# Kernel tuning notes

Hardware: AMD Instinct MI355X
Metric: run time of the kernel (lower is better)

Reference implementation:

```python
import math
import jax, jax.numpy as jnp
import numpy as np

B, C, H, W = 8, 128, 128, 128

def _cosine_basis(n):
    pos = (jnp.arange(n, dtype=jnp.float32) + 0.5) / n          # [n]
    freq = jnp.arange(n, dtype=jnp.float32)[:, None]            # [n,1]
    basis = jnp.cos(freq * pos[None, :] * math.pi) * math.sqrt(2.0 / n)
    return basis.at[0, :].multiply(1.0 / math.sqrt(2.0))        # [n,n]


def setup_inputs() -> dict:
    key = jax.random.key(0)
    ks = jax.random.split(key, 12)
    s = 0.02
    return {
        "x":        jax.random.normal(ks[0], (B, C, H, W), jnp.float32),
        "dw_w":     jax.random.normal(ks[1], (C, 1, 3, 3), jnp.float32) * s,
        "dw_b":     jnp.zeros((C,), jnp.float32),
        "in_w":     jax.random.normal(ks[2], (2 * C, C), jnp.float32) * s,
        "in_b":     jnp.zeros((2 * C,), jnp.float32),
        "out_w":    jax.random.normal(ks[3], (C, C), jnp.float32) * s,
        "out_b":    jnp.zeros((C,), jnp.float32),
        "ln_w":     jnp.ones((C,), jnp.float32),
        "ln_b":     jnp.zeros((C,), jnp.float32),
        "ph_w":     jax.random.normal(ks[4], (C, C), jnp.float32) * s,
        "ph_b":     jnp.zeros((C,), jnp.float32),
        "wave_speed": jnp.ones((1,), jnp.float32),
        "damping":    jnp.full((1,), 0.1, jnp.float32),
        "freq_embed": jax.random.normal(ks[5], (H, W, C), jnp.float32) * s,
    }


def reference(x, dw_w, dw_b, in_w, in_b, out_w, out_b, ln_w, ln_b,
              ph_w, ph_b, wave_speed, damping, freq_embed):
    # depthwise 3x3 conv (groups=C), padding=1
    mixed = jax.lax.conv_general_dilated(
        x, dw_w, window_strides=(1, 1), padding=((1, 1), (1, 1)),
        dimension_numbers=("NCHW", "OIHW", "NCHW"), feature_group_count=C)
    mixed = mixed + dw_b[None, :, None, None]
    mixed = jnp.transpose(mixed, (0, 2, 3, 1))                  # [B,H,W,C]

    proj = mixed @ in_w.T + in_b                                # [B,H,W,2C]
    carrier, gate = jnp.split(proj, 2, axis=-1)

    cos_h = _cosine_basis(H)
    cos_w = _cosine_basis(W)
    # DCT-II along H then W
    spectral = jnp.einsum("bhwc,nh->bnwc", carrier, cos_h)
    spectral = jnp.einsum("bnwc,mw->bnmc", spectral, cos_w)     # [B,H,W,C] (freq)

    # phase modulation (base_resolution == H == W, so no resize)
    phase = jax.nn.gelu(freq_embed @ ph_w.T + ph_b, approximate=False)  # [H,W,C]
    wave_phase = wave_speed * phase                             # broadcast [H,W,C]
    vel_scale = jnp.sin(wave_phase) / jnp.maximum(jnp.abs(wave_speed), 1e-6)
    modulated = (jnp.cos(wave_phase) + vel_scale * (1.0 + 0.5 * damping)) * spectral

    # inverse DCT
    fused = jnp.einsum("bnmc,wm->bnwc", modulated, cos_w.T)
    fused = jnp.einsum("bnwc,hn->bhwc", fused, cos_h.T)         # [B,H,W,C]

    # LayerNorm over channels
    mu = jnp.mean(fused, axis=-1, keepdims=True)
    var = jnp.mean(jnp.square(fused - mu), axis=-1, keepdims=True)
    fused = (fused - mu) / jnp.sqrt(var + 1e-5) * ln_w + ln_b

    fused = fused * jax.nn.silu(gate)
    out = fused @ out_w.T + out_b                               # [B,H,W,C]
    return jnp.transpose(out, (0, 3, 1, 2))                     # [B,C,H,W]
```

## Files before the change

### kernel.cpp

```cpp
#include <hip/hip_runtime.h>
#include <math.h>

#ifndef M_PI
#define M_PI 3.14159265358979323846
#endif

typedef float fx4 __attribute__((ext_vector_type(4)));
typedef __bf16 bf16x8 __attribute__((ext_vector_type(8)));
typedef __bf16 bf16x4 __attribute__((ext_vector_type(4)));

__device__ __forceinline__ unsigned short f2bf(float f){
  union { float f; unsigned u; } v; v.f = f;
  unsigned r = v.u + 0x7FFFu + ((v.u >> 16) & 1u);
  return (unsigned short)(r >> 16);
}
__device__ __forceinline__ float bf2f(unsigned short u){
  union { unsigned u; float f; } v; v.u = ((unsigned)u) << 16;
  return v.f;
}
__device__ __forceinline__ int swz(int row, int colbyte){
  return row*256 + (colbyte ^ ((row & 7) << 4));
}

template<typename FA, typename FB>
__device__ __forceinline__ void run_gemm(FA la, FB lb, fx4 (&acc)[4][4]){
  bf16x8 a[2][4], b[2][4];
  #pragma unroll
  for (int mi=0;mi<4;mi++){ a[0][mi]=la(mi,0); b[0][mi]=lb(mi,0); }
  #pragma unroll
  for (int ks=0; ks<4; ks++){
    int cur = ks&1, nxt = cur^1;
    if (ks<3){
      #pragma unroll
      for (int mi=0;mi<4;mi++){ a[nxt][mi]=la(mi,ks+1); b[nxt][mi]=lb(mi,ks+1); }
    }
    #pragma unroll
    for (int mi=0;mi<4;mi++)
      #pragma unroll
      for (int ni=0;ni<4;ni++)
        acc[mi][ni] = __builtin_amdgcn_mfma_f32_16x16x32_bf16(a[cur][mi], b[cur][ni], acc[mi][ni], 0, 0, 0);
  }
}

template<typename FA0, typename FA1, typename FB>
__device__ __forceinline__ void run_pair_sharedB(FA0 la0, FA1 la1, FB lb,
                                                 fx4 (&acc0)[4][4], fx4 (&acc1)[4][4]){
  bf16x8 a0[2][4], a1[2][4], b[2][4];
  #pragma unroll
  for (int mi=0;mi<4;mi++){ a0[0][mi]=la0(mi,0); a1[0][mi]=la1(mi,0); b[0][mi]=lb(mi,0); }
  #pragma unroll
  for (int ks=0; ks<4; ks++){
    int cur = ks&1, nxt = cur^1;
    if (ks<3){
      #pragma unroll
      for (int mi=0;mi<4;mi++){ a0[nxt][mi]=la0(mi,ks+1); a1[nxt][mi]=la1(mi,ks+1); b[nxt][mi]=lb(mi,ks+1); }
    }
    #pragma unroll
    for (int mi=0;mi<4;mi++)
      #pragma unroll
      for (int ni=0;ni<4;ni++){
        acc0[mi][ni] = __builtin_amdgcn_mfma_f32_16x16x32_bf16(a0[cur][mi], b[cur][ni], acc0[mi][ni], 0, 0, 0);
        acc1[mi][ni] = __builtin_amdgcn_mfma_f32_16x16x32_bf16(a1[cur][mi], b[cur][ni], acc1[mi][ni], 0, 0, 0);
      }
  }
}

template<typename FA, typename FB0, typename FB1>
__device__ __forceinline__ void run_pair_sharedA(FA la, FB0 lb0, FB1 lb1,
                                                 fx4 (&acc0)[4][4], fx4 (&acc1)[4][4]){
  bf16x8 a[2][4], b0[2][4], b1[2][4];
  #pragma unroll
  for (int mi=0;mi<4;mi++){ a[0][mi]=la(mi,0); b0[0][mi]=lb0(mi,0); b1[0][mi]=lb1(mi,0); }
  #pragma unroll
  for (int ks=0; ks<4; ks++){
    int cur = ks&1, nxt = cur^1;
    if (ks<3){
      #pragma unroll
      for (int mi=0;mi<4;mi++){ a[nxt][mi]=la(mi,ks+1); b0[nxt][mi]=lb0(mi,ks+1); b1[nxt][mi]=lb1(mi,ks+1); }
    }
    #pragma unroll
    for (int mi=0;mi<4;mi++)
      #pragma unroll
      for (int ni=0;ni<4;ni++){
        acc0[mi][ni] = __builtin_amdgcn_mfma_f32_16x16x32_bf16(a[cur][mi], b0[cur][ni], acc0[mi][ni], 0, 0, 0);
        acc1[mi][ni] = __builtin_amdgcn_mfma_f32_16x16x32_bf16(a[cur][mi], b1[cur][ni], acc1[mi][ni], 0, 0, 0);
      }
  }
}

__global__ __launch_bounds__(256) void k1_prep_cast_conv(
    const float* __restrict__ in_w, const float* __restrict__ ph_w,
    const float* __restrict__ out_w, const float* __restrict__ fe,
    const float* __restrict__ x, const float* __restrict__ dw_w,
    const float* __restrict__ dw_b,
    unsigned short* __restrict__ basis_bf, unsigned short* __restrict__ basisT_bf,
    unsigned short* __restrict__ ph_w_bf, unsigned short* __restrict__ in_w_bf,
    unsigned short* __restrict__ out_w_bf, unsigned short* __restrict__ feb,
    unsigned short* __restrict__ conv)
{
  int blk = blockIdx.x;
  int t = threadIdx.x;
  if (blk < 128){
    if (t >= 128) return;
    int n = blk, h = t;
    double arg = (double)(n*(2*h+1)) * (M_PI/256.0);
    double v = cos(arg) * 0.125;
    if (n==0) v *= 0.7071067811865476;
    unsigned short bv = f2bf((float)v);
    basis_bf[n*128+h]  = bv;
    basisT_bf[h*128+n] = bv;
    ph_w_bf[n*128+h]  = f2bf(ph_w[n*128+h]);
    in_w_bf[n*128+h]        = f2bf(in_w[n*128+h]);
    in_w_bf[(n+128)*128+h]  = f2bf(in_w[(n+128)*128+h]);
    out_w_bf[n*128+h]       = f2bf(out_w[n*128+h]);
    return;
  }
  if (blk < 1152){
    int idx = (blk-128)*256 + t;
    const float* s = fe + (size_t)idx*8;
    float4 f0 = *(const float4*)s;
    float4 f1 = *(const float4*)(s+4);
    unsigned short o[8];
    o[0]=f2bf(f0.x); o[1]=f2bf(f0.y); o[2]=f2bf(f0.z); o[3]=f2bf(f0.w);
    o[4]=f2bf(f1.x); o[5]=f2bf(f1.y); o[6]=f2bf(f1.z); o[7]=f2bf(f1.w);
    *(int4*)(feb + (size_t)idx*8) = *(const int4*)o;
    return;
  }
  {
    int bb = blk - 1152;
    int plane = bb >> 2, band = bb & 3;
    int c = plane & 127;
    const float* xp = x + (size_t)plane*16384;
    unsigned short* op = conv + (size_t)plane*16384;
    const float* kw = dw_w + c*9;
    float k0=kw[0],k1=kw[1],k2=kw[2],k3=kw[3],k4=kw[4],k5=kw[5],k6=kw[6],k7=kw[7],k8=kw[8];
    float bias = dw_b[c];
    int q = t & 31;
    int w0 = q*4;
    int rg = t >> 5;
    int h0 = band*32 + rg*4;
    bool le = (q==0), re = (q==31);
    float4 fA, fB, fC; float lA,rA,lB,rB,lC,rC;
    #define LOADROW(hh, f, l, r) { \
      int hc = (hh)<0 ? 0 : ((hh)>127 ? 127 : (hh)); \
      f = *(const float4*)(xp + hc*128 + w0); \
      float lu = __shfl_up(f.w, 1, 32); \
      float rd = __shfl_down(f.x, 1, 32); \
      l = le ? 0.f : lu; \
      r = re ? 0.f : rd; \
      if ((hh)<0 || (hh)>127){ f = make_float4(0.f,0.f,0.f,0.f); l=0.f; r=0.f; } \
    }
    LOADROW(h0-1, fA,lA,rA);
    LOADROW(h0,   fB,lB,rB);
    #pragma unroll
    for (int i=0;i<4;i++){
      LOADROW(h0+1+i, fC,lC,rC);
      float4 o;
      o.x = bias; o.y = bias; o.z = bias; o.w = bias;
      o.x = fmaf(k0,lA,  fmaf(k1,fA.x, fmaf(k2,fA.y, o.x)));
      o.y = fmaf(k0,fA.x,fmaf(k1,fA.y, fmaf(k2,fA.z, o.y)));
      o.z = fmaf(k0,fA.y,fmaf(k1,fA.z, fmaf(k2,fA.w, o.z)));
      o.w = fmaf(k0,fA.z,fmaf(k1,fA.w, fmaf(k2,rA,   o.w)));
      o.x = fmaf(k3,lB,  fmaf(k4,fB.x, fmaf(k5,fB.y, o.x)));
      o.y = fmaf(k3,fB.x,fmaf(k4,fB.y, fmaf(k5,fB.z, o.y)));
      o.z = fmaf(k3,fB.y,fmaf(k4,fB.z, fmaf(k5,fB.w, o.z)));
      o.w = fmaf(k3,fB.z,fmaf(k4,fB.w, fmaf(k5,rB,   o.w)));
      o.x = fmaf(k6,lC,  fmaf(k7,fC.x, fmaf(k8,fC.y, o.x)));
      o.y = fmaf(k6,fC.x,fmaf(k7,fC.y, fmaf(k8,fC.z, o.y)));
      o.z = fmaf(k6,fC.y,fmaf(k7,fC.z, fmaf(k8,fC.w, o.z)));
      o.w = fmaf(k6,fC.z,fmaf(k7,fC.w, fmaf(k8,rC,   o.w)));
      bf16x4 v;
      v[0]=(__bf16)o.x; v[1]=(__bf16)o.y; v[2]=(__bf16)o.z; v[3]=(__bf16)o.w;
      *(bf16x4*)(op + (size_t)(h0+i)*128 + w0) = v;
      fA=fB; lA=lB; rA=rB;
      fB=fC; lB=lC; rB=rC;
    }
    #undef LOADROW
  }
}

__global__ __launch_bounds__(512) void k2_inproj_projk(
  const unsigned short* __restrict__ conv, const unsigned short* __restrict__ in_w_bf,
  const float* __restrict__ in_b, unsigned short* __restrict__ carrier,
  unsigned short* __restrict__ gate,
  const unsigned short* __restrict__ feb, const unsigned short* __restrict__ ph_w_bf,
  float* __restrict__ projT)
{
  int blk = blockIdx.x;
  int t = threadIdx.x;
  if (blk >= 1024){
    if (t >= 256) return;
    int r0 = (blk - 1024) * 128;
    int l = t & 63, wid = t >> 6;
    int wm = wid >> 1, wn = wid & 1;
    int lr = l & 15, lk = (l>>4)*8, ld4 = (l>>4)*4;
    fx4 acc[4][4];
    #pragma unroll
    for (int i=0;i<4;i++) for (int j=0;j<4;j++) acc[i][j] = (fx4){0.f,0.f,0.f,0.f};
    run_gemm(
      [&](int mi,int ks)->bf16x8{ return *(const bf16x8*)(feb + (size_t)(r0 + wm*64+mi*16+lr)*128 + ks*32+lk); },
      [&](int ni,int ks)->bf16x8{ return *(const bf16x8*)(ph_w_bf + (size_t)(wn*64+ni*16+lr)*128 + ks*32+lk); },
      acc);
    #pragma unroll
    for (int mi=0;mi<4;mi++)
      #pragma unroll
      for (int ni=0;ni<4;ni++){
        int c = wn*64 + ni*16 + lr;
        int r = r0 + wm*64 + mi*16 + ld4;
        *(fx4*)(projT + (size_t)c*16384 + r) = acc[mi][ni];
      }
    return;
  }
  __shared__ char A[32768];
  int b = blk>>7, h = blk&127;
  const unsigned short* C = conv + (size_t)b*2097152 + h*128;
  {
    int wl = t & 63, grp = t >> 6;
    #pragma unroll
    for (int p=0;p<2;p++){
      int w = wl + 64*p;
      #pragma unroll
      for (int q=0;q<4;q++){
        int c0 = (q*8 + grp)*4;
        ushort4 v;
        v.x = C[(size_t)(c0+0)*16384 + w];
        v.y = C[(size_t)(c0+1)*16384 + w];
        v.z = C[(size_t)(c0+2)*16384 + w];
        v.w = C[(size_t)(c0+3)*16384 + w];
        *(ushort4*)(A + swz(w, c0*2)) = v;
      }
    }
  }
  __syncthreads();
  int l = t & 63, wid = t >> 6;
  int wm = wid >> 2, wn = wid & 3;
  int lr = l & 15, lk = (l>>4)*8, ld4 = (l>>4)*4;
  fx4 acc[4][4];
  #pragma unroll
  for (int i=0;i<4;i++) for (int j=0;j<4;j++) acc[i][j] = (fx4){0.f,0.f,0.f,0.f};
  run_gemm(
    [&](int mi,int ks)->bf16x8{ return *(const bf16x8*)(A + swz(wm*64+mi*16+lr, (ks*32+lk)*2)); },
    [&](int ni,int ks)->bf16x8{ return *(const bf16x8*)(in_w_bf + (size_t)(wn*64+ni*16+lr)*128 + ks*32+lk); },
    acc);
  __syncthreads();
  if (wn < 2){
    #pragma unroll
    for (int mi=0;mi<4;mi++)
      #pragma unroll
      for (int ni=0;ni<4;ni++){
        int n = wn*64 + ni*16 + lr;
        int w0 = wm*64 + mi*16 + ld4;
        float bias = in_b[n];
        bf16x4 v;
        v[0]=(__bf16)(acc[mi][ni][0]+bias); v[1]=(__bf16)(acc[mi][ni][1]+bias);
        v[2]=(__bf16)(acc[mi][ni][2]+bias); v[3]=(__bf16)(acc[mi][ni][3]+bias);
        *(bf16x4*)(carrier + (size_t)(b*128+n)*16384 + h*128 + w0) = v;
      }
  } else {
    #pragma unroll
    for (int mi=0;mi<4;mi++)
      #pragma unroll
      for (int ni=0;ni<4;ni++){
        int n = wn*64 + ni*16 + lr;
        int c = n - 128;
        int w0 = wm*64 + mi*16 + ld4;
        float bias = in_b[n];
        #pragma unroll
        for (int r=0;r<4;r++){
          float v = acc[mi][ni][r] + bias;
          float s = v / (1.0f + __expf(-v));
          *(__bf16*)(A + swz(w0+r, c*2)) = (__bf16)s;
        }
      }
  }
  __syncthreads();
  {
    unsigned short* gout = gate + ((size_t)(b*128+h))*16384;
    int w = t >> 2, cq = (t & 3) * 32;
    #pragma unroll
    for (int i=0;i<4;i++){
      int c0 = cq + i*8;
      int4 v = *(const int4*)(A + swz(w, c0*2));
      *(int4*)(gout + w*128 + c0) = v;
    }
  }
}

__global__ __launch_bounds__(256) void modfin_kernel(
  const float* __restrict__ projT, const float* __restrict__ ph_b,
  const float* __restrict__ wave_speed, const float* __restrict__ damping,
  float* __restrict__ modT)
{
  int blk = blockIdx.x;
  int c = blk >> 4, qb = blk & 15;
  int t = threadIdx.x;
  int q = qb*8 + (t>>5);
  int p0 = (t & 31)*4;
  float ws0 = wave_speed[0];
  float dmp = damping[0];
  float inv = 1.0f / fmaxf(fabsf(ws0), 1e-6f);
  float dampf = 1.0f + 0.5f*dmp;
  float bc = ph_b[c];
  const float* src = projT + (size_t)c*16384 + q;
  float o[4];
  #pragma unroll
  for (int i=0;i<4;i++){
    float v = src[(size_t)(p0+i)*128] + bc;
    float g = 0.5f*v*(1.0f + erff(v*0.70710678118f));
    float wp = ws0*g;
    o[i] = __cosf(wp) + __sinf(wp)*inv*dampf;
  }
  *(float4*)(modT + ((size_t)c*128 + q)*128 + p0) = make_float4(o[0],o[1],o[2],o[3]);
}

__global__ __launch_bounds__(256) void wave_kernel(
  const unsigned short* __restrict__ carrier,
  const unsigned short* __restrict__ basis,
  const unsigned short* __restrict__ basisT,
  const float* __restrict__ modT,
  unsigned short* __restrict__ fused)
{
  __shared__ char U0[32768];
  __shared__ char U1[32768];
  int blk = blockIdx.x;
  int c = blk & 127;
  const unsigned short* X0 = carrier + (size_t)blk*16384;
  const unsigned short* X1 = carrier + (size_t)(blk+512)*16384;
  unsigned short* F0 = fused + (size_t)blk*16384;
  unsigned short* F1 = fused + (size_t)(blk+512)*16384;
  int t = threadIdx.x;
  int l = t & 63, wid = t >> 6;
  int wm = wid >> 1, wn = wid & 1;
  int lr = l & 15, lk = (l>>4)*8, ld4 = (l>>4)*4;
  fx4 acc0[4][4], acc1[4][4];

  #define ZACC { _Pragma("unroll") for (int i=0;i<4;i++) _Pragma("unroll") for (int j=0;j<4;j++){ acc0[i][j]=(fx4){0.f,0.f,0.f,0.f}; acc1[i][j]=(fx4){0.f,0.f,0.f,0.f}; } }
  #define TSTORE(BUF0, BUF1) { \
    _Pragma("unroll") for (int mi=0;mi<4;mi++) \
      _Pragma("unroll") for (int ni=0;ni<4;ni++){ \
        int rr = wn*64 + ni*16 + lr, cc = wm*64 + mi*16 + ld4; \
        bf16x4 v0, v1; \
        v0[0]=(__bf16)acc0[mi][ni][0]; v0[1]=(__bf16)acc0[mi][ni][1]; \
        v0[2]=(__bf16)acc0[mi][ni][2]; v0[3]=(__bf16)acc0[mi][ni][3]; \
        v1[0]=(__bf16)acc1[mi][ni][0]; v1[1]=(__bf16)acc1[mi][ni][1]; \
        v1[2]=(__bf16)acc1[mi][ni][2]; v1[3]=(__bf16)acc1[mi][ni][3]; \
        *(bf16x4*)(BUF0 + swz(rr, cc*2)) = v0; \
        *(bf16x4*)(BUF1 + swz(rr, cc*2)) = v1; \
      } }

  ZACC;
  run_pair_sharedB(
    [&](int mi,int ks)->bf16x8{ return *(const bf16x8*)(X0 + (size_t)(wm*64+mi*16+lr)*128 + ks*32+lk); },
    [&](int mi,int ks)->bf16x8{ return *(const bf16x8*)(X1 + (size_t)(wm*64+mi*16+lr)*128 + ks*32+lk); },
    [&](int ni,int ks)->bf16x8{ return *(const bf16x8*)(basis + (size_t)(wn*64+ni*16+lr)*128 + ks*32+lk); },
    acc0, acc1);
  TSTORE(U0, U1);
  __syncthreads();

  ZACC;
  run_pair_sharedA(
    [&](int mi,int ks)->bf16x8{ return *(const bf16x8*)(basis + (size_t)(wm*64+mi*16+lr)*128 + ks*32+lk); },
    [&](int ni,int ks)->bf16x8{ return *(const bf16x8*)(U0 + swz(wn*64+ni*16+lr, (ks*32+lk)*2)); },
    [&](int ni,int ks)->bf16x8{ return *(const bf16x8*)(U1 + swz(wn*64+ni*16+lr, (ks*32+lk)*2)); },
    acc0, acc1);
  {
    const float* Mc = modT + (size_t)c*16384;
    #pragma unroll
    for (int mi=0;mi<4;mi++)
      #pragma unroll
      for (int ni=0;ni<4;ni++){
        int n0 = wm*64 + mi*16 + ld4, m = wn*64 + ni*16 + lr;
        fx4 mv = *(const fx4*)(Mc + (size_t)m*128 + n0);
        acc0[mi][ni] *= mv;
        acc1[mi][ni] *= mv;
      }
  }
  __syncthreads();
  TSTORE(U0, U1);
  __syncthreads();

  ZACC;
  run_pair_sharedB(
    [&](int mi,int ks)->bf16x8{ return *(const bf16x8*)(U0 + swz(wm*64+mi*16+lr, (ks*32+lk)*2)); },
    [&](int mi,int ks)->bf16x8{ return *(const bf16x8*)(U1 + swz(wm*64+mi*16+lr, (ks*32+lk)*2)); },
    [&](int ni,int ks)->bf16x8{ return *(const bf16x8*)(basisT + (size_t)(wn*64+ni*16+lr)*128 + ks*32+lk); },
    acc0, acc1);
  __syncthreads();
  TSTORE(U0, U1);
  __syncthreads();

  ZACC;
  run_pair_sharedA(
    [&](int mi,int ks)->bf16x8{ return *(const bf16x8*)(basisT + (size_t)(wm*64+mi*16+lr)*128 + ks*32+lk); },
    [&](int ni,int ks)->bf16x8{ return *(const bf16x8*)(U0 + swz(wn*64+ni*16+lr, (ks*32+lk)*2)); },
    [&](int ni,int ks)->bf16x8{ return *(const bf16x8*)(U1 + swz(wn*64+ni*16+lr, (ks*32+lk)*2)); },
    acc0, acc1);
  #pragma unroll
  for (int mi=0;mi<4;mi++)
    #pragma unroll
    for (int ni=0;ni<4;ni++){
      int hh = wn*64 + ni*16 + lr, w0 = wm*64 + mi*16 + ld4;
      bf16x4 v0, v1;
      v0[0]=(__bf16)acc0[mi][ni][0]; v0[1]=(__bf16)acc0[mi][ni][1];
      v0[2]=(__bf16)acc0[mi][ni][2]; v0[3]=(__bf16)acc0[mi][ni][3];
      v1[0]=(__bf16)acc1[mi][ni][0]; v1[1]=(__bf16)acc1[mi][ni][1];
      v1[2]=(__bf16)acc1[mi][ni][2]; v1[3]=(__bf16)acc1[mi][ni][3];
      *(bf16x4*)(F0 + hh*128 + w0) = v0;
      *(bf16x4*)(F1 + hh*128 + w0) = v1;
    }
  #undef ZACC
  #undef TSTORE
}

__global__ __launch_bounds__(256) void final_kernel(
  const unsigned short* __restrict__ fused, const unsigned short* __restrict__ gate,
  const unsigned short* __restrict__ out_w_bf, const float* __restrict__ out_b,
  const float* __restrict__ ln_w, const float* __restrict__ ln_b,
  float* __restrict__ out)
{
  __shared__ char Fl[32768];
  __shared__ char Al[32768];
  __shared__ float red[256], red2[256];
  __shared__ float mu[128], rs[128];
  int blk = blockIdx.x; int b = blk>>7, h = blk&127;
  const unsigned short* Fsrc = fused + (size_t)b*2097152 + h*128;
  const unsigned short* G = gate + (size_t)blk*16384;
  int t = threadIdx.x;
  {
    int c = t>>1, wq = (t&1)*64;
    #pragma unroll
    for (int i=0;i<8;i++){
      int w0 = wq + i*8;
      int4 v = *(const int4*)(Fsrc + (size_t)c*16384 + w0);
      *(int4*)(Fl + swz(c, w0*2)) = v;
    }
  }
  __syncthreads();
  {
    int w = t&127, half = t>>7;
    float s=0.f, q=0.f;
    for (int i=0;i<64;i++){
      int c = half*64 + i;
      float f = bf2f(*(const unsigned short*)(Fl + swz(c, w*2)));
      s += f; q = fmaf(f,f,q);
    }
    red[t]=s; red2[t]=q;
  }
  __syncthreads();
  if (t < 128){
    float ss = red[t]+red[t+128], qq = red2[t]+red2[t+128];
    float m = ss*(1.f/128.f);
    float var = qq*(1.f/128.f) - m*m;
    mu[t]=m; rs[t]=rsqrtf(var+1e-5f);
  }
  __syncthreads();
  {
    int w = t>>1, cq = (t&1)*64;
    float m_ = mu[w], r_ = rs[w];
    #pragma unroll
    for (int i=0;i<8;i++){
      int c0 = cq + i*8;
      ushort4 g0 = *(const ushort4*)(G + (size_t)w*128 + c0);
      ushort4 g1 = *(const ushort4*)(G + (size_t)w*128 + c0 + 4);
      unsigned short ov[8];
      unsigned short gv[8] = {g0.x,g0.y,g0.z,g0.w,g1.x,g1.y,g1.z,g1.w};
      #pragma unroll
      for (int j=0;j<8;j++){
        int cc = c0+j;
        float f = bf2f(*(const unsigned short*)(Fl + swz(cc, w*2)));
        float a = fmaf((f-m_)*r_, ln_w[cc], ln_b[cc]) * bf2f(gv[j]);
        ov[j] = f2bf(a);
      }
      *(int4*)(Al + swz(w, c0*2)) = *(const int4*)ov;
    }
  }
  __syncthreads();
  int l = t & 63, wid = t >> 6;
  int wm = wid >> 1, wn = wid & 1;
  int lr = l & 15, lk = (l>>4)*8, ld4 = (l>>4)*4;
  fx4 acc[4][4];
  #pragma unroll
  for (int i=0;i<4;i++) for (int j=0;j<4;j++) acc[i][j] = (fx4){0.f,0.f,0.f,0.f};
  run_gemm(
    [&](int mi,int ks)->bf16x8{ return *(const bf16x8*)(Al + swz(wm*64+mi*16+lr, (ks*32+lk)*2)); },
    [&](int ni,int ks)->bf16x8{ return *(const bf16x8*)(out_w_bf + (size_t)(wn*64+ni*16+lr)*128 + ks*32+lk); },
    acc);
  #pragma unroll
  for (int mi=0;mi<4;mi++)
    #pragma unroll
    for (int ni=0;ni<4;ni++){
      int j = wn*64 + ni*16 + lr, w0 = wm*64 + mi*16 + ld4;
      float bj = out_b[j];
      fx4 o = acc[mi][ni];
      o[0]+=bj; o[1]+=bj; o[2]+=bj; o[3]+=bj;
      *(fx4*)(out + ((size_t)(b*128 + j)*128 + h)*128 + w0) = o;
    }
}

extern "C" void kernel_launch(void* const* d_in, const int* in_sizes, int n_in,
                              void* d_out, int out_size, void* d_ws, size_t ws_size,
                              hipStream_t stream)
{
  const float* x      = (const float*)d_in[0];
  const float* dw_w   = (const float*)d_in[1];
  const float* dw_b   = (const float*)d_in[2];
  const float* in_w   = (const float*)d_in[3];
  const float* in_b   = (const float*)d_in[4];
  const float* out_w  = (const float*)d_in[5];
  const float* out_b  = (const float*)d_in[6];
  const float* ln_w   = (const float*)d_in[7];
  const float* ln_b   = (const float*)d_in[8];
  const float* ph_w   = (const float*)d_in[9];
  const float* ph_b   = (const float*)d_in[10];
  const float* wsp    = (const float*)d_in[11];
  const float* dmp    = (const float*)d_in[12];
  const float* fe     = (const float*)d_in[13];
  float* outp = (float*)d_out;

  float* modT  = (float*)d_ws;
  float* projT = modT + 2097152;
  unsigned short* feb      = (unsigned short*)(projT + 2097152);
  unsigned short* conv     = feb     + 2097152;
  unsigned short* carrier  = conv    + 16777216;
  unsigned short* gate     = carrier + 16777216;
  unsigned short* fusedb   = gate    + 16777216;
  unsigned short* basis_bf = fusedb  + 16777216;
  unsigned short* basisT_bf= basis_bf + 16384;
  unsigned short* in_w_bf  = basisT_bf + 16384;
  unsigned short* out_w_bf = in_w_bf + 32768;
  unsigned short* ph_w_bf  = out_w_bf + 16384;

  k1_prep_cast_conv<<<5248,256,0,stream>>>(in_w, ph_w, out_w, fe, x, dw_w, dw_b,
      basis_bf, basisT_bf, ph_w_bf, in_w_bf, out_w_bf, feb, conv);
  k2_inproj_projk<<<1152,512,0,stream>>>(conv, in_w_bf, in_b, carrier, gate,
      feb, ph_w_bf, projT);
  modfin_kernel<<<2048,256,0,stream>>>(projT, ph_b, wsp, dmp, modT);
  wave_kernel<<<512,256,0,stream>>>(carrier, basis_bf, basisT_bf, modT, fusedb);
  final_kernel<<<1024,256,0,stream>>>(fusedb, gate, out_w_bf, out_b, ln_w, ln_b, outp);
}
```

Measured before the change: 157.0 us.

## Fuse phase projection GEMM into conv kernel and modfin into in-proj kernel

The phase-projection GEMM now reads fp32 freq_embed and ph_w directly and converts them to bf16 in registers, which removes the separate feb/ph_w bf16 cast pass and its intermediate buffer. That GEMM moves into the first kernel as extra blocks. The modulation (GELU/sin/cos) work moves into the second kernel as extra blocks, removing one kernel launch. The cost is that fp32 loads in the GEMM fetch twice the bytes of bf16, and the fused blocks share launch resources with unrelated work.

```diff
diff --git a/kernel.cpp b/kernel.cpp
--- a/kernel.cpp
+++ b/kernel.cpp
@@ -21,6 +21,14 @@
 __device__ __forceinline__ int swz(int row, int colbyte){
   return row*256 + (colbyte ^ ((row & 7) << 4));
 }
+__device__ __forceinline__ bf16x8 f8tobf(const float* p){
+  float4 a = *(const float4*)p;
+  float4 b = *(const float4*)(p+4);
+  bf16x8 r;
+  r[0]=(__bf16)a.x; r[1]=(__bf16)a.y; r[2]=(__bf16)a.z; r[3]=(__bf16)a.w;
+  r[4]=(__bf16)b.x; r[5]=(__bf16)b.y; r[6]=(__bf16)b.z; r[7]=(__bf16)b.w;
+  return r;
+}
 
 template<typename FA, typename FB>
 __device__ __forceinline__ void run_gemm(FA la, FB lb, fx4 (&acc)[4][4]){
@@ -88,15 +96,14 @@
   }
 }
 
-__global__ __launch_bounds__(256) void k1_prep_cast_conv(
+__global__ __launch_bounds__(256) void k1_prep_conv_projk(
     const float* __restrict__ in_w, const float* __restrict__ ph_w,
     const float* __restrict__ out_w, const float* __restrict__ fe,
     const float* __restrict__ x, const float* __restrict__ dw_w,
     const float* __restrict__ dw_b,
     unsigned short* __restrict__ basis_bf, unsigned short* __restrict__ basisT_bf,
-    unsigned short* __restrict__ ph_w_bf, unsigned short* __restrict__ in_w_bf,
-    unsigned short* __restrict__ out_w_bf, unsigned short* __restrict__ feb,
-    unsigned short* __restrict__ conv)
+    unsigned short* __restrict__ in_w_bf, unsigned short* __restrict__ out_w_bf,
+    unsigned short* __restrict__ conv, float* __restrict__ projT)
 {
   int blk = blockIdx.x;
   int t = threadIdx.x;
@@ -109,25 +116,35 @@
     unsigned short bv = f2bf((float)v);
     basis_bf[n*128+h]  = bv;
     basisT_bf[h*128+n] = bv;
-    ph_w_bf[n*128+h]  = f2bf(ph_w[n*128+h]);
     in_w_bf[n*128+h]        = f2bf(in_w[n*128+h]);
     in_w_bf[(n+128)*128+h]  = f2bf(in_w[(n+128)*128+h]);
     out_w_bf[n*128+h]       = f2bf(out_w[n*128+h]);
     return;
   }
-  if (blk < 1152){
-    int idx = (blk-128)*256 + t;
-    const float* s = fe + (size_t)idx*8;
-    float4 f0 = *(const float4*)s;
-    float4 f1 = *(const float4*)(s+4);
-    unsigned short o[8];
-    o[0]=f2bf(f0.x); o[1]=f2bf(f0.y); o[2]=f2bf(f0.z); o[3]=f2bf(f0.w);
-    o[4]=f2bf(f1.x); o[5]=f2bf(f1.y); o[6]=f2bf(f1.z); o[7]=f2bf(f1.w);
-    *(int4*)(feb + (size_t)idx*8) = *(const int4*)o;
+  if (blk >= 4224){
+    int r0 = (blk - 4224) * 128;
+    int l = t & 63, wid = t >> 6;
+    int wm = wid >> 1, wn = wid & 1;
+    int lr = l & 15, lk = (l>>4)*8, ld4 = (l>>4)*4;
+    fx4 acc[4][4];
+    #pragma unroll
+    for (int i=0;i<4;i++) for (int j=0;j<4;j++) acc[i][j] = (fx4){0.f,0.f,0.f,0.f};
+    run_gemm(
+      [&](int mi,int ks)->bf16x8{ return f8tobf(fe + (size_t)(r0 + wm*64+mi*16+lr)*128 + ks*32+lk); },
+      [&](int ni,int ks)->bf16x8{ return f8tobf(ph_w + (size_t)(wn*64+ni*16+lr)*128 + ks*32+lk); },
+      acc);
+    #pragma unroll
+    for (int mi=0;mi<4;mi++)
+      #pragma unroll
+      for (int ni=0;ni<4;ni++){
+        int c = wn*64 + ni*16 + lr;
+        int r = r0 + wm*64 + mi*16 + ld4;
+        *(fx4*)(projT + (size_t)c*16384 + r) = acc[mi][ni];
+      }
     return;
   }
   {
-    int bb = blk - 1152;
+    int bb = blk - 128;
     int plane = bb >> 2, band = bb & 3;
     int c = plane & 127;
     const float* xp = x + (size_t)plane*16384;
@@ -179,36 +196,37 @@
   }
 }
 
-__global__ __launch_bounds__(512) void k2_inproj_projk(
+__global__ __launch_bounds__(512) void k2_inproj_modfin(
   const unsigned short* __restrict__ conv, const unsigned short* __restrict__ in_w_bf,
   const float* __restrict__ in_b, unsigned short* __restrict__ carrier,
   unsigned short* __restrict__ gate,
-  const unsigned short* __restrict__ feb, const unsigned short* __restrict__ ph_w_bf,
-  float* __restrict__ projT)
+  const float* __restrict__ projT, const float* __restrict__ ph_b,
+  const float* __restrict__ wave_speed, const float* __restrict__ damping,
+  float* __restrict__ modT)
 {
   int blk = blockIdx.x;
   int t = threadIdx.x;
   if (blk >= 1024){
-    if (t >= 256) return;
-    int r0 = (blk - 1024) * 128;
-    int l = t & 63, wid = t >> 6;
-    int wm = wid >> 1, wn = wid & 1;
-    int lr = l & 15, lk = (l>>4)*8, ld4 = (l>>4)*4;
-    fx4 acc[4][4];
-    #pragma unroll
-    for (int i=0;i<4;i++) for (int j=0;j<4;j++) acc[i][j] = (fx4){0.f,0.f,0.f,0.f};
-    run_gemm(
-      [&](int mi,int ks)->bf16x8{ return *(const bf16x8*)(feb + (size_t)(r0 + wm*64+mi*16+lr)*128 + ks*32+lk); },
-      [&](int ni,int ks)->bf16x8{ return *(const bf16x8*)(ph_w_bf + (size_t)(wn*64+ni*16+lr)*128 + ks*32+lk); },
-      acc);
-    #pragma unroll
-    for (int mi=0;mi<4;mi++)
-      #pragma unroll
-      for (int ni=0;ni<4;ni++){
-        int c = wn*64 + ni*16 + lr;
-        int r = r0 + wm*64 + mi*16 + ld4;
-        *(fx4*)(projT + (size_t)c*16384 + r) = acc[mi][ni];
-      }
+    int mblk = (blk - 1024)*2 + (t >= 256 ? 1 : 0);
+    int tt = t & 255;
+    int c = mblk >> 4, qb = mblk & 15;
+    int q = qb*8 + (tt>>5);
+    int p0 = (tt & 31)*4;
+    float ws0 = wave_speed[0];
+    float dmp = damping[0];
+    float inv = 1.0f / fmaxf(fabsf(ws0), 1e-6f);
+    float dampf = 1.0f + 0.5f*dmp;
+    float bc = ph_b[c];
+    const float* src = projT + (size_t)c*16384 + q;
+    float o[4];
+    #pragma unroll
+    for (int i=0;i<4;i++){
+      float v = src[(size_t)(p0+i)*128] + bc;
+      float g = 0.5f*v*(1.0f + erff(v*0.70710678118f));
+      float wp = ws0*g;
+      o[i] = __cosf(wp) + __sinf(wp)*inv*dampf;
+    }
+    *(float4*)(modT + ((size_t)c*128 + q)*128 + p0) = make_float4(o[0],o[1],o[2],o[3]);
     return;
   }
   __shared__ char A[32768];
@@ -284,33 +302,6 @@
       *(int4*)(gout + w*128 + c0) = v;
     }
   }
-}
-
-__global__ __launch_bounds__(256) void modfin_kernel(
-  const float* __restrict__ projT, const float* __restrict__ ph_b,
-  const float* __restrict__ wave_speed, const float* __restrict__ damping,
-  float* __restrict__ modT)
-{
-  int blk = blockIdx.x;
-  int c = blk >> 4, qb = blk & 15;
-  int t = threadIdx.x;
-  int q = qb*8 + (t>>5);
-  int p0 = (t & 31)*4;
-  float ws0 = wave_speed[0];
-  float dmp = damping[0];
-  float inv = 1.0f / fmaxf(fabsf(ws0), 1e-6f);
-  float dampf = 1.0f + 0.5f*dmp;
-  float bc = ph_b[c];
-  const float* src = projT + (size_t)c*16384 + q;
-  float o[4];
-  #pragma unroll
-  for (int i=0;i<4;i++){
-    float v = src[(size_t)(p0+i)*128] + bc;
-    float g = 0.5f*v*(1.0f + erff(v*0.70710678118f));
-    float wp = ws0*g;
-    o[i] = __cosf(wp) + __sinf(wp)*inv*dampf;
-  }
-  *(float4*)(modT + ((size_t)c*128 + q)*128 + p0) = make_float4(o[0],o[1],o[2],o[3]);
 }
 
 __global__ __launch_bounds__(256) void wave_kernel(
@@ -519,8 +510,7 @@
 
   float* modT  = (float*)d_ws;
   float* projT = modT + 2097152;
-  unsigned short* feb      = (unsigned short*)(projT + 2097152);
-  unsigned short* conv     = feb     + 2097152;
+  unsigned short* conv     = (unsigned short*)(projT + 2097152);
   unsigned short* carrier  = conv    + 16777216;
   unsigned short* gate     = carrier + 16777216;
   unsigned short* fusedb   = gate    + 16777216;
@@ -528,13 +518,11 @@
   unsigned short* basisT_bf= basis_bf + 16384;
   unsigned short* in_w_bf  = basisT_bf + 16384;
   unsigned short* out_w_bf = in_w_bf + 32768;
-  unsigned short* ph_w_bf  = out_w_bf + 16384;
-
-  k1_prep_cast_conv<<<5248,256,0,stream>>>(in_w, ph_w, out_w, fe, x, dw_w, dw_b,
-      basis_bf, basisT_bf, ph_w_bf, in_w_bf, out_w_bf, feb, conv);
-  k2_inproj_projk<<<1152,512,0,stream>>>(conv, in_w_bf, in_b, carrier, gate,
-      feb, ph_w_bf, projT);
-  modfin_kernel<<<2048,256,0,stream>>>(projT, ph_b, wsp, dmp, modT);
+
+  k1_prep_conv_projk<<<4352,256,0,stream>>>(in_w, ph_w, out_w, fe, x, dw_w, dw_b,
+      basis_bf, basisT_bf, in_w_bf, out_w_bf, conv, projT);
+  k2_inproj_modfin<<<2048,512,0,stream>>>(conv, in_w_bf, in_b, carrier, gate,
+      projT, ph_b, wsp, dmp, modT);
   wave_kernel<<<512,256,0,stream>>>(carrier, basis_bf, basisT_bf, modT, fusedb);
   final_kernel<<<1024,256,0,stream>>>(fusedb, gate, out_w_bf, out_b, ln_w, ln_b, outp);
 }
```

Measured after the change: 181.4 us. 1.16x slower.
